# Kernel tuning notes

Measured on AMD Instinct MI355X. Metric: run time of the kernel, lower is better.

The kernel has to match this reference:

```python
import jax, jax.numpy as jnp
import numpy as np

B, R, L = 1, 128, 256
IN_DIM, DM, DIM = 128, 32, 128  # in_dim, dim_msa, dim


def setup_inputs() -> dict:
    key = jax.random.key(0)
    k = jax.random.split(key, 6)
    x = jax.random.normal(k[0], (B, L, L, DIM), dtype=jnp.float32)
    m = jax.random.normal(k[1], (B, R, L, IN_DIM), dtype=jnp.float32)
    # proj_down1: Linear(in_dim -> dim_msa)
    W1 = jax.random.normal(k[2], (DM, IN_DIM), dtype=jnp.float32) * (1.0 / np.sqrt(IN_DIM))
    b1 = jax.random.normal(k[3], (DM,), dtype=jnp.float32) * 0.02
    # proj_down2: Linear(dim_msa**2 -> dim)
    W2 = jax.random.normal(k[4], (DIM, DM * DM), dtype=jnp.float32) * (1.0 / DM)
    b2 = jax.random.normal(k[5], (DIM,), dtype=jnp.float32) * 0.02
    return {"x": x, "m": m, "W1": W1, "b1": b1, "W2": W2, "b2": b2}


def reference(x, m, W1, b1, W2, b2):
    # proj_down1: [b, r, i, in_dim] -> [b, r, i, dim_msa]
    mp = jnp.einsum('brie,de->brid', m, W1) + b1
    nrows = mp.shape[1]
    # Original math: outer = einsum('brid,brjc->bijcd', mp, mp)/nrows,
    # then rearrange 'b i j c d -> b i j (c d)' and Linear(dm^2 -> dim).
    # Flattened index (c d) => W2[k, c*DM + d]; fuse projection into the
    # contraction so the huge [b,i,j,c,d] tensor is never materialized.
    W2r = W2.reshape(DIM, DM, DM)  # (k, c, d)
    outer = jnp.einsum('brid,brjc,kcd->bijk', mp, mp, W2r) / nrows + b2
    return x + outer
```

## Files before the change

### kernel.cpp

```cpp
#include <hip/hip_runtime.h>
#include <stdint.h>


typedef __attribute__((ext_vector_type(8))) short bf16x8;
typedef __attribute__((ext_vector_type(4))) float f32x4;

#define MFMA16 __builtin_amdgcn_mfma_f32_16x16x32_bf16

__device__ __forceinline__ unsigned short f2bf(float f) {
    union { float f; unsigned int u; } x; x.f = f;
    unsigned int r = (x.u + 0x7fffu + ((x.u >> 16) & 1u)) >> 16;
    return (unsigned short)r;
}

__device__ __forceinline__ bf16x8 load8f_bf(const float* p) {
    float4 v0 = *(const float4*)p;
    float4 v1 = *(const float4*)(p + 4);
    union { bf16x8 v; unsigned short u[8]; } r;
    r.u[0] = f2bf(v0.x); r.u[1] = f2bf(v0.y); r.u[2] = f2bf(v0.z); r.u[3] = f2bf(v0.w);
    r.u[4] = f2bf(v1.x); r.u[5] = f2bf(v1.y); r.u[6] = f2bf(v1.z); r.u[7] = f2bf(v1.w);
    return r.v;
}

__global__ __launch_bounds__(256) void prep_kernel(
    const float* __restrict__ m, const float* __restrict__ W1,
    const float* __restrict__ pb1, const float* __restrict__ W2,
    unsigned short* __restrict__ mpF, unsigned short* __restrict__ W2f)
{
    const int bx = blockIdx.x;
    if (bx >= 512) {
        const int t    = (bx - 512) * 256 + threadIdx.x;
        const int nt   = t >> 11;
        const int kc   = (t >> 6) & 31;
        const int lane = t & 63;
        const int ln   = lane & 15, q = lane >> 4;
        const float* src = W2 + (size_t)(nt * 16 + ln) * 1024 + kc;
        union { bf16x8 v; unsigned short u[8]; } r;
        #pragma unroll
        for (int j = 0; j < 8; ++j)
            r.u[j] = f2bf(src[(q * 8 + j) * 32]);
        *(bf16x8*)(W2f + (size_t)t * 8) = r.v;
        return;
    }
    const int lane = threadIdx.x & 63;
    const int w    = threadIdx.x >> 6;
    const int ln   = lane & 15, q = lane >> 4;
    const int tile = bx * 4 + w;
    const int i    = tile >> 3;
    const int r0   = (tile & 7) * 16;

    const float* Ap  = m  + ((size_t)(r0 + ln) * 256 + i) * 128 + q * 8;
    const float* Bp0 = W1 + (size_t)ln * 128 + q * 8;
    const float* Bp1 = W1 + (size_t)(16 + ln) * 128 + q * 8;

    f32x4 acc0 = {0.f, 0.f, 0.f, 0.f};
    f32x4 acc1 = {0.f, 0.f, 0.f, 0.f};
    #pragma unroll
    for (int ke = 0; ke < 4; ++ke) {
        bf16x8 a  = load8f_bf(Ap  + ke * 32);
        bf16x8 b0 = load8f_bf(Bp0 + ke * 32);
        bf16x8 b1 = load8f_bf(Bp1 + ke * 32);
        acc0 = MFMA16(a, b0, acc0, 0, 0, 0);
        acc1 = MFMA16(a, b1, acc1, 0, 0, 0);
    }
    const float bb0 = pb1[ln];
    const float bb1 = pb1[16 + ln];
    const int kr = r0 >> 5;
    const int qr = ((r0 >> 4) & 1) * 2 + (q >> 1);
    const int j0 = (q & 1) * 4;
    const size_t off0 = (size_t)(i * 2 + 0) * 2048 + kr * 512 + (qr * 16 + ln) * 8 + j0;
    const size_t off1 = (size_t)(i * 2 + 1) * 2048 + kr * 512 + (qr * 16 + ln) * 8 + j0;
    ushort4 o0, o1;
    o0.x = f2bf(acc0[0] + bb0); o0.y = f2bf(acc0[1] + bb0);
    o0.z = f2bf(acc0[2] + bb0); o0.w = f2bf(acc0[3] + bb0);
    o1.x = f2bf(acc1[0] + bb1); o1.y = f2bf(acc1[1] + bb1);
    o1.z = f2bf(acc1[2] + bb1); o1.w = f2bf(acc1[3] + bb1);
    *(ushort4*)(mpF + off0) = o0;
    *(ushort4*)(mpF + off1) = o1;
}

__device__ __forceinline__ void stage_load(const unsigned short* __restrict__ mpF,
                                           int i0, int dhalf, int tid, uint4 (&stg)[4])
{
    #pragma unroll
    for (int r = 0; r < 4; ++r) {
        const int cid = r * 512 + tid;
        const int it  = cid >> 8;
        const int pos = cid & 255;
        stg[r] = *(const uint4*)(mpF + (size_t)((i0 + it) * 2 + dhalf) * 2048 + pos * 8);
    }
}

__device__ __forceinline__ void stage_store(unsigned short* __restrict__ Bs,
                                            int tid, const uint4 (&stg)[4])
{
    #pragma unroll
    for (int r = 0; r < 4; ++r) {
        const int cid = r * 512 + tid;
        const int it  = cid >> 8;
        const int pos = cid & 255;
        *(uint4*)(Bs + it * 2048 + pos * 8) = stg[r];
    }
}

__device__ __forceinline__ void stepB(const unsigned short* __restrict__ Ab,
                                      const unsigned short* __restrict__ Bs,
                                      int wn, int lane, f32x4 (&acc)[2][4])
{
    #pragma unroll
    for (int a = 0; a < 2; ++a)
        #pragma unroll
        for (int b = 0; b < 4; ++b)
            acc[a][b] = (f32x4){0.f, 0.f, 0.f, 0.f};
    #pragma unroll
    for (int ks = 0; ks < 4; ++ks) {
        bf16x8 av[2], bv[4];
        av[0] = *(const bf16x8*)(Ab + ks * 512);
        av[1] = *(const bf16x8*)(Ab + 2048 + ks * 512);
        #pragma unroll
        for (int bn = 0; bn < 4; ++bn)
            bv[bn] = *(const bf16x8*)(Bs + (wn * 4 + bn) * 2048 + ks * 512 + lane * 8);
        #pragma unroll
        for (int am = 0; am < 2; ++am)
            #pragma unroll
            for (int bn = 0; bn < 4; ++bn)
                acc[am][bn] = MFMA16(av[am], bv[bn], acc[am][bn], 0, 0, 0);
    }
}

__device__ __forceinline__ void gwrite(unsigned short* __restrict__ Gl,
                                       const f32x4 (&acc)[2][4],
                                       int ln, int q, int wm, int wn)
{
    #pragma unroll
    for (int am = 0; am < 2; ++am) {
        const int chunk = ln * 4 + am * 2 + (q >> 1);
        const int sig   = chunk >> 3;
        const int hbase = chunk * 256 + (q & 1) * 4;
        #pragma unroll
        for (int bn = 0; bn < 4; ++bn) {
            const int p  = (wn * 4 + bn) * 4 + wm;
            const int pp = p ^ sig;
            ushort4 g;
            g.x = f2bf(acc[am][bn][0]); g.y = f2bf(acc[am][bn][1]);
            g.z = f2bf(acc[am][bn][2]); g.w = f2bf(acc[am][bn][3]);
            *(ushort4*)(Gl + hbase + pp * 8) = g;
        }
    }
}

__device__ __forceinline__ void wpre(const unsigned short* __restrict__ wp, bf16x8 (&wv)[8])
{
    #pragma unroll
    for (int k8 = 0; k8 < 8; ++k8)
        wv[k8] = *(const bf16x8*)(wp + k8 * 512);
}

__device__ __forceinline__ void stepC(const unsigned short* __restrict__ Gl,
                                      const unsigned short* __restrict__ wp,
                                      bf16x8 (&wv)[8], int ln, int q,
                                      f32x4& c0, f32x4& c1)
{
    #pragma unroll
    for (int ks = 0; ks < 16; ++ks) {
        bf16x8 cur = wv[ks & 7];
        if (ks < 8) wv[ks & 7] = *(const bf16x8*)(wp + (ks + 8) * 512);
        const int chunk = ks * 4 + q;
        const int sig   = chunk >> 3;
        const unsigned short* gp = Gl + chunk * 256 + ((ln ^ sig) << 3);
        bf16x8 ag0 = *(const bf16x8*)gp;
        bf16x8 ag1 = *(const bf16x8*)(gp + 128);
        c0 = MFMA16(ag0, cur, c0, 0, 0, 0);
        c1 = MFMA16(ag1, cur, c1, 0, 0, 0);
    }
}

__global__ __launch_bounds__(512, 4) void fused_kernel(
    const float* __restrict__ x, const float* __restrict__ b2,
    const unsigned short* __restrict__ mpF, const unsigned short* __restrict__ W2f,
    float* __restrict__ out)
{
    __shared__ __align__(16) unsigned char smem[65536];
    unsigned short* Gl = (unsigned short*)smem;
    unsigned short* Bs = (unsigned short*)(smem + 32768);

    const int tid  = threadIdx.x;
    const int lane = tid & 63, w = tid >> 6;
    const int ln   = lane & 15, q = lane >> 4;
    const int wm   = w & 3, wn = w >> 2;

    const int i0 = blockIdx.x * 8;
    const int j0 = blockIdx.y * 8;

    const unsigned short* Ab0 = mpF + (size_t)((j0 + wm) * 2) * 2048 + lane * 8;
    const unsigned short* Ab1 = Ab0 + 16384;
    const unsigned short* wp0 = W2f + (size_t)(w * 32) * 512 + lane * 8;
    const unsigned short* wp1 = wp0 + 16 * 512;

    f32x4 cacc[4];
    #pragma unroll
    for (int t = 0; t < 4; ++t) cacc[t] = (f32x4){0.f, 0.f, 0.f, 0.f};
    f32x4 acc[2][4];
    bf16x8 wv[8];
    uint4 stg[4];

    stage_load(mpF, i0, 0, tid, stg);
    stage_store(Bs, tid, stg);
    __syncthreads();

    stepB(Ab0, Bs, wn, lane, acc);
    wpre(wp0, wv);
    gwrite(Gl, acc, ln, q, wm, wn);
    __syncthreads();
    stepC(Gl, wp0, wv, ln, q, cacc[0], cacc[1]);

    stepB(Ab1, Bs, wn, lane, acc);
    __syncthreads();
    wpre(wp0, wv);
    gwrite(Gl, acc, ln, q, wm, wn);
    __syncthreads();
    stage_load(mpF, i0, 1, tid, stg);
    stepC(Gl, wp0, wv, ln, q, cacc[2], cacc[3]);
    stage_store(Bs, tid, stg);
    __syncthreads();

    stepB(Ab0, Bs, wn, lane, acc);
    wpre(wp1, wv);
    gwrite(Gl, acc, ln, q, wm, wn);
    __syncthreads();
    stepC(Gl, wp1, wv, ln, q, cacc[0], cacc[1]);

    stepB(Ab1, Bs, wn, lane, acc);
    __syncthreads();
    wpre(wp1, wv);
    gwrite(Gl, acc, ln, q, wm, wn);
    __syncthreads();

    float4 xv[4];
    size_t gb[4];
    #pragma unroll
    for (int e = 0; e < 4; ++e) {
        const int fid = e * 512 + tid;
        const int po  = fid >> 5, kq = fid & 31;
        gb[e] = ((size_t)(i0 + (po >> 3)) * 256 + (j0 + (po & 7))) * 128 + kq * 4;
        xv[e] = *(const float4*)(x + gb[e]);
    }

    stepC(Gl, wp1, wv, ln, q, cacc[2], cacc[3]);
    __syncthreads();

    float* Ep = (float*)smem;
    const float invR = 1.0f / 128.0f;
    const int kk = w * 16 + ln;
    const int u  = kk >> 2, kl = kk & 3;
    #pragma unroll
    for (int jh = 0; jh < 2; ++jh)
        #pragma unroll
        for (int pt = 0; pt < 2; ++pt)
            #pragma unroll
            for (int rg = 0; rg < 4; ++rg) {
                const int po = (pt * 4 + q) * 8 + jh * 4 + rg;
                Ep[po * 128 + ((u ^ (po & 7)) << 2) + kl] = cacc[jh * 2 + pt][rg] * invR;
            }
    __syncthreads();

    #pragma unroll
    for (int e = 0; e < 4; ++e) {
        const int fid = e * 512 + tid;
        const int po  = fid >> 5, kq = fid & 31;
        const float4 v  = *(const float4*)(Ep + po * 128 + ((kq ^ (po & 7)) << 2));
        const float4 bv = *(const float4*)(b2 + kq * 4);
        float4 o;
        o.x = xv[e].x + v.x + bv.x; o.y = xv[e].y + v.y + bv.y;
        o.z = xv[e].z + v.z + bv.z; o.w = xv[e].w + v.w + bv.w;
        *(float4*)(out + gb[e]) = o;
    }
}

extern "C" void kernel_launch(void* const* d_in, const int* in_sizes, int n_in,
                              void* d_out, int out_size, void* d_ws, size_t ws_size,
                              hipStream_t stream) {
    const float* x  = (const float*)d_in[0];
    const float* m  = (const float*)d_in[1];
    const float* W1 = (const float*)d_in[2];
    const float* b1 = (const float*)d_in[3];
    const float* W2 = (const float*)d_in[4];
    const float* b2 = (const float*)d_in[5];
    float* out = (float*)d_out;

    unsigned short* mpF = (unsigned short*)d_ws;
    unsigned short* W2f = mpF + (size_t)512 * 2048;

    prep_kernel<<<dim3(576), dim3(256), 0, stream>>>(m, W1, b1, W2, mpF, W2f);
    fused_kernel<<<dim3(32, 32), dim3(512), 0, stream>>>(x, b2, mpF, W2f, out);
}
```

Before: 138.4 us.

## Repartition warp tiling: split contraction K across warp halves and reduce in LDS

Changes the warp layout so stage-B warps compute 4x2 MFMA tiles with A fragments loaded straight from global memory. Stage C is split along the K dimension between two warp halves, and each warp produces two output-column tiles per A fragment. The two halves combine their partial sums through an extra LDS pass and a barrier. The intent is to reuse the LDS-loaded G fragments across two W2 tiles and to shorten each warp's serial K loop. The cost is more global A loads, an extra synchronization, and a leftover dead helper function (stepB6).

```diff
diff --git a/kernel.cpp b/kernel.cpp
--- a/kernel.cpp
+++ b/kernel.cpp
@@ -103,43 +103,73 @@
     }
 }
 
-__device__ __forceinline__ void stepB(const unsigned short* __restrict__ Ab,
-                                      const unsigned short* __restrict__ Bs,
-                                      int wn, int lane, f32x4 (&acc)[2][4])
-{
-    #pragma unroll
-    for (int a = 0; a < 2; ++a)
-        #pragma unroll
-        for (int b = 0; b < 4; ++b)
+__device__ __forceinline__ void stepB6(const unsigned short* __restrict__ mpF,
+                                       const unsigned short* __restrict__ Bs,
+                                       int j0, int jh, int wm, int wn, int lane,
+                                       f32x4 (&acc)[4][2])
+{
+    #pragma unroll
+    for (int a = 0; a < 4; ++a)
+        #pragma unroll
+        for (int b = 0; b < 2; ++b)
             acc[a][b] = (f32x4){0.f, 0.f, 0.f, 0.f};
     #pragma unroll
     for (int ks = 0; ks < 4; ++ks) {
-        bf16x8 av[2], bv[4];
-        av[0] = *(const bf16x8*)(Ab + ks * 512);
-        av[1] = *(const bf16x8*)(Ab + 2048 + ks * 512);
-        #pragma unroll
-        for (int bn = 0; bn < 4; ++bn)
-            bv[bn] = *(const bf16x8*)(Bs + (wn * 4 + bn) * 2048 + ks * 512 + lane * 8);
-        #pragma unroll
-        for (int am = 0; am < 2; ++am)
+        bf16x8 av[4], bv[2];
+        #pragma unroll
+        for (int am = 0; am < 4; ++am) {
+            const int rt = (j0 + jh * 4 + wm * 2 + (am >> 1)) * 2 + (am & 1);
+            av[am] = *(const bf16x8*)(mpF + (size_t)rt * 2048 + ks * 512 + lane * 8);
+        }
+        #pragma unroll
+        for (int bn = 0; bn < 2; ++bn)
+            bv[bn] = *(const bf16x8*)(Bs + (lane & 512 ? 0 : 0) + ((0) ) + ( ( ( (bn) + 0) ) * 0 ) + ( ( ( ( (0) ) ) ) ) + ( ( ( ( ( ( (int)0 ) ) ) ) ) ) + ( ( ( ( ( ( ( ( (int)((0)) ) ) ) ) ) ) ) ) + ( ( ( ( ( ( ( (0) ) ) ) ) ) ) ) + ( ( ( ( (0) ) ) ) ) + ( ( ( (0) ) ) ) + ( ( (0) ) ) + ( (0) ) + (0) + ( ( ( ( ( ( ( ( ( (0) ) ) ) ) ) ) ) ) ) + 0 );
+        (void)bv;
+        break;
+    }
+}
+
+__device__ __forceinline__ void stepB6r(const unsigned short* __restrict__ mpF,
+                                        const unsigned short* __restrict__ Bs,
+                                        int j0, int jh, int wm, int wn, int lane,
+                                        f32x4 (&acc)[4][2])
+{
+    #pragma unroll
+    for (int a = 0; a < 4; ++a)
+        #pragma unroll
+        for (int b = 0; b < 2; ++b)
+            acc[a][b] = (f32x4){0.f, 0.f, 0.f, 0.f};
+    #pragma unroll
+    for (int ks = 0; ks < 4; ++ks) {
+        bf16x8 av[4], bv[2];
+        #pragma unroll
+        for (int am = 0; am < 4; ++am) {
+            const int rt = (j0 + jh * 4 + wm * 2 + (am >> 1)) * 2 + (am & 1);
+            av[am] = *(const bf16x8*)(mpF + (size_t)rt * 2048 + ks * 512 + lane * 8);
+        }
+        #pragma unroll
+        for (int bn = 0; bn < 2; ++bn)
+            bv[bn] = *(const bf16x8*)(Bs + (wn * 2 + bn) * 2048 + ks * 512 + lane * 8);
+        #pragma unroll
+        for (int am = 0; am < 4; ++am)
             #pragma unroll
-            for (int bn = 0; bn < 4; ++bn)
+            for (int bn = 0; bn < 2; ++bn)
                 acc[am][bn] = MFMA16(av[am], bv[bn], acc[am][bn], 0, 0, 0);
     }
 }
 
-__device__ __forceinline__ void gwrite(unsigned short* __restrict__ Gl,
-                                       const f32x4 (&acc)[2][4],
-                                       int ln, int q, int wm, int wn)
-{
-    #pragma unroll
-    for (int am = 0; am < 2; ++am) {
-        const int chunk = ln * 4 + am * 2 + (q >> 1);
+__device__ __forceinline__ void gwrite6(unsigned short* __restrict__ Gl,
+                                        const f32x4 (&acc)[4][2],
+                                        int ln, int q, int wm, int wn)
+{
+    #pragma unroll
+    for (int am = 0; am < 4; ++am) {
+        const int chunk = ln * 4 + (am & 1) * 2 + (q >> 1);
         const int sig   = chunk >> 3;
         const int hbase = chunk * 256 + (q & 1) * 4;
         #pragma unroll
-        for (int bn = 0; bn < 4; ++bn) {
-            const int p  = (wn * 4 + bn) * 4 + wm;
+        for (int bn = 0; bn < 2; ++bn) {
+            const int p  = (wn * 2 + bn) * 4 + wm * 2 + (am >> 1);
             const int pp = p ^ sig;
             ushort4 g;
             g.x = f2bf(acc[am][bn][0]); g.y = f2bf(acc[am][bn][1]);
@@ -149,29 +179,30 @@
     }
 }
 
-__device__ __forceinline__ void wpre(const unsigned short* __restrict__ wp, bf16x8 (&wv)[8])
-{
-    #pragma unroll
-    for (int k8 = 0; k8 < 8; ++k8)
-        wv[k8] = *(const bf16x8*)(wp + k8 * 512);
-}
-
-__device__ __forceinline__ void stepC(const unsigned short* __restrict__ Gl,
-                                      const unsigned short* __restrict__ wp,
-                                      bf16x8 (&wv)[8], int ln, int q,
-                                      f32x4& c0, f32x4& c1)
-{
-    #pragma unroll
-    for (int ks = 0; ks < 16; ++ks) {
-        bf16x8 cur = wv[ks & 7];
-        if (ks < 8) wv[ks & 7] = *(const bf16x8*)(wp + (ks + 8) * 512);
-        const int chunk = ks * 4 + q;
-        const int sig   = chunk >> 3;
+__device__ __forceinline__ void stepC6(const unsigned short* __restrict__ Gl,
+                                       const unsigned short* __restrict__ wpA,
+                                       const unsigned short* __restrict__ wpB,
+                                       int h, int ln, int q,
+                                       f32x4& c00, f32x4& c01, f32x4& c10, f32x4& c11)
+{
+    bf16x8 wa = *(const bf16x8*)wpA;
+    bf16x8 wb = *(const bf16x8*)wpB;
+    #pragma unroll
+    for (int ks = 0; ks < 8; ++ks) {
+        const int chunk = h * 32 + ks * 4 + q;
+        const int sig   = h * 4 + (ks >> 1);
         const unsigned short* gp = Gl + chunk * 256 + ((ln ^ sig) << 3);
         bf16x8 ag0 = *(const bf16x8*)gp;
         bf16x8 ag1 = *(const bf16x8*)(gp + 128);
-        c0 = MFMA16(ag0, cur, c0, 0, 0, 0);
-        c1 = MFMA16(ag1, cur, c1, 0, 0, 0);
+        bf16x8 ca = wa, cb = wb;
+        if (ks < 7) {
+            wa = *(const bf16x8*)(wpA + (ks + 1) * 512);
+            wb = *(const bf16x8*)(wpB + (ks + 1) * 512);
+        }
+        c00 = MFMA16(ag0, ca, c00, 0, 0, 0);
+        c10 = MFMA16(ag1, ca, c10, 0, 0, 0);
+        c01 = MFMA16(ag0, cb, c01, 0, 0, 0);
+        c11 = MFMA16(ag1, cb, c11, 0, 0, 0);
     }
 }
 
@@ -187,53 +218,57 @@
     const int tid  = threadIdx.x;
     const int lane = tid & 63, w = tid >> 6;
     const int ln   = lane & 15, q = lane >> 4;
-    const int wm   = w & 3, wn = w >> 2;
+    const int wm   = w & 1, wn = (w >> 1) & 3;
+    const int h    = w >> 2;
+    const int kt4  = w & 3;
 
     const int i0 = blockIdx.x * 8;
     const int j0 = blockIdx.y * 8;
 
-    const unsigned short* Ab0 = mpF + (size_t)((j0 + wm) * 2) * 2048 + lane * 8;
-    const unsigned short* Ab1 = Ab0 + 16384;
-    const unsigned short* wp0 = W2f + (size_t)(w * 32) * 512 + lane * 8;
-    const unsigned short* wp1 = wp0 + 16 * 512;
-
-    f32x4 cacc[4];
-    #pragma unroll
-    for (int t = 0; t < 4; ++t) cacc[t] = (f32x4){0.f, 0.f, 0.f, 0.f};
-    f32x4 acc[2][4];
-    bf16x8 wv[8];
+    f32x4 cacc[2][2][2];
+    #pragma unroll
+    for (int a = 0; a < 2; ++a)
+        #pragma unroll
+        for (int b = 0; b < 2; ++b)
+            #pragma unroll
+            for (int c = 0; c < 2; ++c)
+                cacc[a][b][c] = (f32x4){0.f, 0.f, 0.f, 0.f};
+
+    f32x4 acc[4][2];
     uint4 stg[4];
+
+    const unsigned short* wA0 = W2f + (size_t)((kt4 * 2) * 32 + h * 8) * 512 + lane * 8;
+    const unsigned short* wB0 = wA0 + (size_t)32 * 512;
+    const unsigned short* wA1 = wA0 + (size_t)16 * 512;
+    const unsigned short* wB1 = wB0 + (size_t)16 * 512;
 
     stage_load(mpF, i0, 0, tid, stg);
     stage_store(Bs, tid, stg);
     __syncthreads();
 
-    stepB(Ab0, Bs, wn, lane, acc);
-    wpre(wp0, wv);
-    gwrite(Gl, acc, ln, q, wm, wn);
-    __syncthreads();
-    stepC(Gl, wp0, wv, ln, q, cacc[0], cacc[1]);
-
-    stepB(Ab1, Bs, wn, lane, acc);
-    __syncthreads();
-    wpre(wp0, wv);
-    gwrite(Gl, acc, ln, q, wm, wn);
+    stepB6r(mpF, Bs, j0, 0, wm, wn, lane, acc);
+    gwrite6(Gl, acc, ln, q, wm, wn);
+    __syncthreads();
+    stepC6(Gl, wA0, wB0, h, ln, q,
+           cacc[0][0][0], cacc[0][0][1], cacc[0][1][0], cacc[0][1][1]);
+    stepB6r(mpF, Bs, j0, 1, wm, wn, lane, acc);
+    __syncthreads();
+    gwrite6(Gl, acc, ln, q, wm, wn);
     __syncthreads();
     stage_load(mpF, i0, 1, tid, stg);
-    stepC(Gl, wp0, wv, ln, q, cacc[2], cacc[3]);
+    stepC6(Gl, wA0, wB0, h, ln, q,
+           cacc[1][0][0], cacc[1][0][1], cacc[1][1][0], cacc[1][1][1]);
     stage_store(Bs, tid, stg);
     __syncthreads();
 
-    stepB(Ab0, Bs, wn, lane, acc);
-    wpre(wp1, wv);
-    gwrite(Gl, acc, ln, q, wm, wn);
-    __syncthreads();
-    stepC(Gl, wp1, wv, ln, q, cacc[0], cacc[1]);
-
-    stepB(Ab1, Bs, wn, lane, acc);
-    __syncthreads();
-    wpre(wp1, wv);
-    gwrite(Gl, acc, ln, q, wm, wn);
+    stepB6r(mpF, Bs, j0, 0, wm, wn, lane, acc);
+    gwrite6(Gl, acc, ln, q, wm, wn);
+    __syncthreads();
+    stepC6(Gl, wA1, wB1, h, ln, q,
+           cacc[0][0][0], cacc[0][0][1], cacc[0][1][0], cacc[0][1][1]);
+    stepB6r(mpF, Bs, j0, 1, wm, wn, lane, acc);
+    __syncthreads();
+    gwrite6(Gl, acc, ln, q, wm, wn);
     __syncthreads();
 
     float4 xv[4];
@@ -246,22 +281,45 @@
         xv[e] = *(const float4*)(x + gb[e]);
     }
 
-    stepC(Gl, wp1, wv, ln, q, cacc[2], cacc[3]);
+    stepC6(Gl, wA1, wB1, h, ln, q,
+           cacc[1][0][0], cacc[1][0][1], cacc[1][1][0], cacc[1][1][1]);
     __syncthreads();
 
     float* Ep = (float*)smem;
     const float invR = 1.0f / 128.0f;
-    const int kk = w * 16 + ln;
-    const int u  = kk >> 2, kl = kk & 3;
-    #pragma unroll
-    for (int jh = 0; jh < 2; ++jh)
-        #pragma unroll
-        for (int pt = 0; pt < 2; ++pt)
+    if (h == 0) {
+        #pragma unroll
+        for (int jh = 0; jh < 2; ++jh)
             #pragma unroll
-            for (int rg = 0; rg < 4; ++rg) {
-                const int po = (pt * 4 + q) * 8 + jh * 4 + rg;
-                Ep[po * 128 + ((u ^ (po & 7)) << 2) + kl] = cacc[jh * 2 + pt][rg] * invR;
-            }
+            for (int pg = 0; pg < 2; ++pg)
+                #pragma unroll
+                for (int kt = 0; kt < 2; ++kt)
+                    #pragma unroll
+                    for (int rg = 0; rg < 4; ++rg) {
+                        const int po  = (pg * 4 + q) * 8 + jh * 4 + rg;
+                        const int col = (kt4 * 2 + kt) * 16 + ln;
+                        const int u   = col >> 2;
+                        Ep[po * 128 + ((u ^ (po & 7)) << 2) + (col & 3)] =
+                            cacc[jh][pg][kt][rg] * invR;
+                    }
+    }
+    __syncthreads();
+    if (h == 1) {
+        #pragma unroll
+        for (int jh = 0; jh < 2; ++jh)
+            #pragma unroll
+            for (int pg = 0; pg < 2; ++pg)
+                #pragma unroll
+                for (int kt = 0; kt < 2; ++kt)
+                    #pragma unroll
+                    for (int rg = 0; rg < 4; ++rg) {
+                        const int po  = (pg * 4 + q) * 8 + jh * 4 + rg;
+                        const int col = (kt4 * 2 + kt) * 16 + ln;
+                        const int u   = col >> 2;
+                        Ep[po * 128 + ((u ^ (po & 7)) << 2) + (col & 3)] +=
+                            cacc[jh][pg][kt][rg] * invR;
+                    }
+    }
     __syncthreads();
 
     #pragma unroll
```

Result: slower. 146.1 us (+5.5%).
